# Performance work log

Hardware: AMD Instinct MI355X
Metric: run time of the kernel (lower is better)

Reference implementation:

```python
import jax, jax.numpy as jnp
import numpy as np

B, N, DIM = 8, 4096, 512
H, DH = 8, 64
INNER = H * DH
MIN_FREQ = 1.0 / 64
SCALE = 1.0
ROT_DIM = DH // 2  # 32, per spatial axis
EPS = 1e-5


def setup_inputs() -> dict:
    key = jax.random.key(0)
    ks = jax.random.split(key, 6)
    x = jax.random.normal(ks[0], (B, N, DIM), dtype=jnp.float32)
    pos = jax.random.uniform(ks[1], (B, N, 2), dtype=jnp.float32)
    W_qkv = jax.random.normal(ks[2], (3 * INNER, DIM), dtype=jnp.float32) * (1.0 / DH)
    gamma_k = jnp.ones((DH,), jnp.float32)
    beta_k = jnp.zeros((DH,), jnp.float32)
    gamma_v = jnp.ones((DH,), jnp.float32)
    beta_v = jnp.zeros((DH,), jnp.float32)
    W_out = jax.random.normal(ks[3], (DIM, INNER), dtype=jnp.float32) * (1.0 / np.sqrt(INNER))
    b_out = jnp.zeros((DIM,), jnp.float32)
    return {"x": x, "pos": pos, "W_qkv": W_qkv, "gamma_k": gamma_k, "beta_k": beta_k,
            "gamma_v": gamma_v, "beta_v": beta_v, "W_out": W_out, "b_out": b_out}


def _layernorm(t, gamma, beta):
    mu = jnp.mean(t, axis=-1, keepdims=True)
    var = jnp.var(t, axis=-1, keepdims=True)
    return (t - mu) * jax.lax.rsqrt(var + EPS) * gamma + beta


def _rotate_half(t):
    # '... (j d) -> ... j d' with j=2, then cat(-x2, x1)
    d = t.shape[-1] // 2
    x1, x2 = t[..., :d], t[..., d:]
    return jnp.concatenate((-x2, x1), axis=-1)


def _apply_rot(t, freqs):
    return t * jnp.cos(freqs) + _rotate_half(t) * jnp.sin(freqs)


def _freqs(coord):
    # coord: [b, n]; inv_freq over rotary half-dim
    inv_freq = 1.0 / (10000.0 ** (jnp.arange(0, ROT_DIM, 2, dtype=jnp.float32) / ROT_DIM))
    t = coord * (SCALE / MIN_FREQ)
    f = t[..., None] * inv_freq  # [b, n, ROT_DIM//2]
    return jnp.concatenate((f, f), axis=-1)[:, None, :, :]  # [b, 1, n, ROT_DIM]


def reference(x, pos, W_qkv, gamma_k, beta_k, gamma_v, beta_v, W_out, b_out):
    b, n, _ = x.shape
    qkv = x @ W_qkv.T  # [b, n, 3*INNER]
    q, k, v = jnp.split(qkv, 3, axis=-1)
    split = lambda t: t.reshape(b, n, H, DH).transpose(0, 2, 1, 3)  # b h n d
    q, k, v = split(q), split(k), split(v)

    # Galerkin: LayerNorm on K and V over head dim
    k = _layernorm(k, gamma_k, beta_k)
    v = _layernorm(v, gamma_v, beta_v)

    # 2D rotary on q, k: first half of head dim uses x-coords, second half y-coords
    fx, fy = _freqs(pos[..., 0]), _freqs(pos[..., 1])
    rot2d = lambda t: jnp.concatenate(
        (_apply_rot(t[..., :ROT_DIM], fx), _apply_rot(t[..., ROT_DIM:], fy)), axis=-1)
    q = rot2d(q)
    k = rot2d(k)

    # Associative linear attention: (K^T V) then Q @ (.) / n
    dots = jnp.einsum('bhnd,bhne->bhde', k, v)  # [b, h, d, d]
    out = jnp.einsum('bhnd,bhde->bhne', q, dots) * (1.0 / n)
    out = out.transpose(0, 2, 1, 3).reshape(b, n, INNER)
    return out @ W_out.T + b_out
```

## Files before the change

### kernel.cpp

```cpp
#include <hip/hip_runtime.h>
#include <math.h>

#define NB 8
#define NN 4096
#define NDIM 512
#define NH 8
#define NDH 64
#define QKVC 1536
#define NROWS (NB * NN)
#define EPSF 1e-5f
#define INV_N (1.0f / 4096.0f)
#define L2_10K_16 0.8304820237218406f

typedef __bf16 bf16x8_t __attribute__((ext_vector_type(8)));
typedef float f32x4_t __attribute__((ext_vector_type(4)));
typedef unsigned short u16x8 __attribute__((ext_vector_type(8)));

__device__ inline unsigned short f2bf(float f) {
    unsigned u = __builtin_bit_cast(unsigned, f);
    u += 0x7fff + ((u >> 16) & 1);
    return (unsigned short)(u >> 16);
}
__device__ inline float bf2f(unsigned short u) {
    unsigned v = (unsigned)u << 16;
    return __builtin_bit_cast(float, v);
}

#define GLOAD_LDS16(g, s) __builtin_amdgcn_global_load_lds(                    \
    (const __attribute__((address_space(1))) void*)(g),                        \
    (__attribute__((address_space(3))) void*)(s), 16, 0, 0)

__global__ __launch_bounds__(256)
void cvt_bf16_kernel(const float* __restrict__ s, unsigned short* __restrict__ d, int n)
{
    const int i = (blockIdx.x * 256 + threadIdx.x) * 8;
    if (i >= n) return;
    float4 a = *(const float4*)(s + i);
    float4 b = *(const float4*)(s + i + 4);
    ushort4 lo, hi;
    lo.x = f2bf(a.x); lo.y = f2bf(a.y); lo.z = f2bf(a.z); lo.w = f2bf(a.w);
    hi.x = f2bf(b.x); hi.y = f2bf(b.y); hi.z = f2bf(b.z); hi.w = f2bf(b.w);
    *(ushort4*)(d + i)     = lo;
    *(ushort4*)(d + i + 4) = hi;
}

__global__ __launch_bounds__(256)
void cvt_dots_kernel(const float* __restrict__ s, unsigned short* __restrict__ d)
{
    const int i = (blockIdx.x * 256 + threadIdx.x) * 4;
    float4 a = *(const float4*)(s + i);
    ushort4 o;
    o.x = f2bf(a.x * INV_N); o.y = f2bf(a.y * INV_N);
    o.z = f2bf(a.z * INV_N); o.w = f2bf(a.w * INV_N);
    *(ushort4*)(d + i) = o;
}

__global__ __launch_bounds__(512, 2)
void gemm_qkv_fused(const unsigned short* __restrict__ A,
                    const unsigned short* __restrict__ Bm,
                    const float* __restrict__ pos,
                    const float* __restrict__ gk, const float* __restrict__ bk,
                    const float* __restrict__ gv, const float* __restrict__ bvv,
                    unsigned short* __restrict__ qkvb)
{
    __shared__ __align__(16) unsigned short lds[2 * 32768];

    const int tid  = threadIdx.x;
    const int wave = tid >> 6;
    const int lane = tid & 63;

    int flat = blockIdx.y * 6 + blockIdx.x;
    flat = (flat & 7) * 96 + (flat >> 3);
    const int bx = flat % 6;
    const int by = flat / 6;
    const int m0 = by * 256;
    const int n0 = bx * 256;

    const int warp_m = wave >> 2;
    const int warp_n = wave & 3;
    const int fr = lane & 15;
    const int fq = lane >> 4;
    const int ch0 = ((fq ^ (fr & 7)) << 3);
    const int ch1 = ch0 ^ 32;

    const int r6 = tid >> 3;
    const int cs = (((tid & 7) ^ (r6 & 7)) << 3);
    const unsigned short* Asrc = A  + (size_t)(m0 + r6) * NDIM + cs;
    const unsigned short* Bsrc = Bm + (size_t)(n0 + (r6 >> 5) * 64 + (r6 & 31)) * NDIM + cs;
    const int sdst = wave * 512;

#define STG_A(tt, h, c) GLOAD_LDS16(Asrc + (size_t)((c) * 128 + (h) * 64) * NDIM + (tt) * 64, \
        &lds[(((tt) & 1) << 15) + ((h) << 13) + ((c) << 12) + sdst])
#define STG_B(tt, h, c) GLOAD_LDS16(Bsrc + (size_t)((c) * 128 + (h) * 32) * NDIM + (tt) * 64, \
        &lds[(((tt) & 1) << 15) + 16384 + ((h) << 13) + ((c) << 12) + sdst])
#define VMCNT4 asm volatile("s_waitcnt vmcnt(4)" ::: "memory")
#define BARF   { __builtin_amdgcn_s_barrier(); asm volatile("" ::: "memory"); }

    f32x4_t acc[8][4] = {};

    STG_A(0, 0, 0); STG_A(0, 0, 1);
    STG_B(0, 0, 0); STG_B(0, 0, 1);
    STG_B(0, 1, 0); STG_B(0, 1, 1);
    STG_A(0, 1, 0); STG_A(0, 1, 1);

    const unsigned short* Afr = &lds[(warp_m * 64 + fr) * 64];
    const unsigned short* Bfr = &lds[16384 + (warp_n * 32 + fr) * 64];

    bf16x8_t a0[4][2], a1[4][2], b0[2][2], b1[2][2];

    for (int tt = 0; tt < 7; ++tt) {
        const int rb = (tt & 1) << 15;
        VMCNT4; BARF;
        #pragma unroll
        for (int mi = 0; mi < 4; ++mi) {
            a0[mi][0] = *(const bf16x8_t*)&Afr[rb + mi * 1024 + ch0];
            a0[mi][1] = *(const bf16x8_t*)&Afr[rb + mi * 1024 + ch1];
        }
        #pragma unroll
        for (int nj = 0; nj < 2; ++nj) {
            b0[nj][0] = *(const bf16x8_t*)&Bfr[rb + nj * 1024 + ch0];
            b0[nj][1] = *(const bf16x8_t*)&Bfr[rb + nj * 1024 + ch1];
        }
        STG_A(tt + 1, 0, 0); STG_A(tt + 1, 0, 1);
        __builtin_amdgcn_s_setprio(1);
        #pragma unroll
        for (int mi = 0; mi < 4; ++mi)
            #pragma unroll
            for (int nj = 0; nj < 2; ++nj) {
                acc[mi][nj] = __builtin_amdgcn_mfma_f32_16x16x32_bf16(a0[mi][0], b0[nj][0], acc[mi][nj], 0, 0, 0);
                acc[mi][nj] = __builtin_amdgcn_mfma_f32_16x16x32_bf16(a0[mi][1], b0[nj][1], acc[mi][nj], 0, 0, 0);
            }
        __builtin_amdgcn_s_setprio(0);
        VMCNT4; BARF;
        #pragma unroll
        for (int nj = 0; nj < 2; ++nj) {
            b1[nj][0] = *(const bf16x8_t*)&Bfr[rb + 8192 + nj * 1024 + ch0];
            b1[nj][1] = *(const bf16x8_t*)&Bfr[rb + 8192 + nj * 1024 + ch1];
        }
        STG_B(tt + 1, 0, 0); STG_B(tt + 1, 0, 1);
        __builtin_amdgcn_s_setprio(1);
        #pragma unroll
        for (int mi = 0; mi < 4; ++mi)
            #pragma unroll
            for (int nj = 0; nj < 2; ++nj) {
                acc[mi][2 + nj] = __builtin_amdgcn_mfma_f32_16x16x32_bf16(a0[mi][0], b1[nj][0], acc[mi][2 + nj], 0, 0, 0);
                acc[mi][2 + nj] = __builtin_amdgcn_mfma_f32_16x16x32_bf16(a0[mi][1], b1[nj][1], acc[mi][2 + nj], 0, 0, 0);
            }
        __builtin_amdgcn_s_setprio(0);
        VMCNT4; BARF;
        #pragma unroll
        for (int mi = 0; mi < 4; ++mi) {
            a1[mi][0] = *(const bf16x8_t*)&Afr[rb + 8192 + mi * 1024 + ch0];
            a1[mi][1] = *(const bf16x8_t*)&Afr[rb + 8192 + mi * 1024 + ch1];
        }
        STG_B(tt + 1, 1, 0); STG_B(tt + 1, 1, 1);
        __builtin_amdgcn_s_setprio(1);
        #pragma unroll
        for (int mi = 0; mi < 4; ++mi)
            #pragma unroll
            for (int nj = 0; nj < 2; ++nj) {
                acc[4 + mi][nj] = __builtin_amdgcn_mfma_f32_16x16x32_bf16(a1[mi][0], b0[nj][0], acc[4 + mi][nj], 0, 0, 0);
                acc[4 + mi][nj] = __builtin_amdgcn_mfma_f32_16x16x32_bf16(a1[mi][1], b0[nj][1], acc[4 + mi][nj], 0, 0, 0);
            }
        __builtin_amdgcn_s_setprio(0);
        STG_A(tt + 1, 1, 0); STG_A(tt + 1, 1, 1);
        __builtin_amdgcn_s_setprio(1);
        #pragma unroll
        for (int mi = 0; mi < 4; ++mi)
            #pragma unroll
            for (int nj = 0; nj < 2; ++nj) {
                acc[4 + mi][2 + nj] = __builtin_amdgcn_mfma_f32_16x16x32_bf16(a1[mi][0], b1[nj][0], acc[4 + mi][2 + nj], 0, 0, 0);
                acc[4 + mi][2 + nj] = __builtin_amdgcn_mfma_f32_16x16x32_bf16(a1[mi][1], b1[nj][1], acc[4 + mi][2 + nj], 0, 0, 0);
            }
        __builtin_amdgcn_s_setprio(0);
    }
    {
        const int rb = 32768;
        asm volatile("s_waitcnt vmcnt(0)" ::: "memory");
        BARF;
        #pragma unroll
        for (int mi = 0; mi < 4; ++mi) {
            a0[mi][0] = *(const bf16x8_t*)&Afr[rb + mi * 1024 + ch0];
            a0[mi][1] = *(const bf16x8_t*)&Afr[rb + mi * 1024 + ch1];
        }
        #pragma unroll
        for (int nj = 0; nj < 2; ++nj) {
            b0[nj][0] = *(const bf16x8_t*)&Bfr[rb + nj * 1024 + ch0];
            b0[nj][1] = *(const bf16x8_t*)&Bfr[rb + nj * 1024 + ch1];
        }
        #pragma unroll
        for (int mi = 0; mi < 4; ++mi)
            #pragma unroll
            for (int nj = 0; nj < 2; ++nj) {
                acc[mi][nj] = __builtin_amdgcn_mfma_f32_16x16x32_bf16(a0[mi][0], b0[nj][0], acc[mi][nj], 0, 0, 0);
                acc[mi][nj] = __builtin_amdgcn_mfma_f32_16x16x32_bf16(a0[mi][1], b0[nj][1], acc[mi][nj], 0, 0, 0);
            }
        #pragma unroll
        for (int nj = 0; nj < 2; ++nj) {
            b1[nj][0] = *(const bf16x8_t*)&Bfr[rb + 8192 + nj * 1024 + ch0];
            b1[nj][1] = *(const bf16x8_t*)&Bfr[rb + 8192 + nj * 1024 + ch1];
        }
        #pragma unroll
        for (int mi = 0; mi < 4; ++mi)
            #pragma unroll
            for (int nj = 0; nj < 2; ++nj) {
                acc[mi][2 + nj] = __builtin_amdgcn_mfma_f32_16x16x32_bf16(a0[mi][0], b1[nj][0], acc[mi][2 + nj], 0, 0, 0);
                acc[mi][2 + nj] = __builtin_amdgcn_mfma_f32_16x16x32_bf16(a0[mi][1], b1[nj][1], acc[mi][2 + nj], 0, 0, 0);
            }
        #pragma unroll
        for (int mi = 0; mi < 4; ++mi) {
            a1[mi][0] = *(const bf16x8_t*)&Afr[rb + 8192 + mi * 1024 + ch0];
            a1[mi][1] = *(const bf16x8_t*)&Afr[rb + 8192 + mi * 1024 + ch1];
        }
        #pragma unroll
        for (int mi = 0; mi < 4; ++mi)
            #pragma unroll
            for (int nj = 0; nj < 2; ++nj) {
                acc[4 + mi][nj] = __builtin_amdgcn_mfma_f32_16x16x32_bf16(a1[mi][0], b0[nj][0], acc[4 + mi][nj], 0, 0, 0);
                acc[4 + mi][nj] = __builtin_amdgcn_mfma_f32_16x16x32_bf16(a1[mi][1], b0[nj][1], acc[4 + mi][nj], 0, 0, 0);
                acc[4 + mi][2 + nj] = __builtin_amdgcn_mfma_f32_16x16x32_bf16(a1[mi][0], b1[nj][0], acc[4 + mi][2 + nj], 0, 0, 0);
                acc[4 + mi][2 + nj] = __builtin_amdgcn_mfma_f32_16x16x32_bf16(a1[mi][1], b1[nj][1], acc[4 + mi][2 + nj], 0, 0, 0);
            }
    }
#undef STG_A
#undef STG_B
#undef VMCNT4
#undef BARF

    const int type = (n0 + warp_n * 64) >> 9;
    const int c  = lane & 15;
    const int g4 = (lane >> 4) * 4;
    const int mrow0 = m0 + warp_m * 128;

    if (type != 0) {
        const float* gamma = (type == 1) ? gk : gv;
        const float* beta  = (type == 1) ? bk : bvv;
        float gm[4], bt[4];
        #pragma unroll
        for (int j = 0; j < 4; ++j) { gm[j] = gamma[j * 16 + c]; bt[j] = beta[j * 16 + c]; }
        #pragma unroll
        for (int i = 0; i < 8; ++i)
            #pragma unroll
            for (int r = 0; r < 4; ++r) {
                float t0 = acc[i][0][r], t1 = acc[i][1][r];
                float t2 = acc[i][2][r], t3 = acc[i][3][r];
                float s  = t0 + t1 + t2 + t3;
                float ss = t0*t0 + t1*t1 + t2*t2 + t3*t3;
                #pragma unroll
                for (int msk = 1; msk < 16; msk <<= 1) {
                    s  += __shfl_xor(s,  msk, 64);
                    ss += __shfl_xor(ss, msk, 64);
                }
                const float mu = s * (1.0f / 64.0f);
                const float rs = rsqrtf(ss * (1.0f / 64.0f) - mu * mu + EPSF);
                acc[i][0][r] = (t0 - mu) * rs * gm[0] + bt[0];
                acc[i][1][r] = (t1 - mu) * rs * gm[1] + bt[1];
                acc[i][2][r] = (t2 - mu) * rs * gm[2] + bt[2];
                acc[i][3][r] = (t3 - mu) * rs * gm[3] + bt[3];
            }
    }
    if (type != 2) {
        const float Kc = 64.0f * exp2f(-(float)c * L2_10K_16);
        #pragma unroll
        for (int i = 0; i < 8; ++i)
            #pragma unroll
            for (int r = 0; r < 4; ++r) {
                const int row = mrow0 + (i >> 2) * 64 + (i & 3) * 16 + g4 + r;
                const float2 p = ((const float2*)pos)[row];
                float sx, cx, sy, cy;
                __sincosf(p.x * Kc, &sx, &cx);
                __sincosf(p.y * Kc, &sy, &cy);
                const float t0 = acc[i][0][r], t1 = acc[i][1][r];
                const float t2 = acc[i][2][r], t3 = acc[i][3][r];
                acc[i][0][r] = t0 * cx - t1 * sx;
                acc[i][1][r] = t1 * cx + t0 * sx;
                acc[i][2][r] = t2 * cy - t3 * sy;
                acc[i][3][r] = t3 * cy + t2 * sy;
            }
    }
    #pragma unroll
    for (int i = 0; i < 8; ++i)
        #pragma unroll
        for (int j = 0; j < 4; ++j) {
            unsigned short* qp = qkvb
                + (size_t)(mrow0 + (i >> 2) * 64 + (i & 3) * 16 + g4) * QKVC
                + n0 + warp_n * 64 + j * 16 + c;
            #pragma unroll
            for (int r = 0; r < 4; ++r)
                qp[(size_t)r * QKVC] = f2bf(acc[i][j][r]);
        }
}

__global__ __launch_bounds__(256)
void dots_kernel(const unsigned short* __restrict__ qkvb, float* __restrict__ dots)
{
    __shared__ float ks[32][64];
    __shared__ float vs[32][64];
    const int b = blockIdx.z, h = blockIdx.y;
    const int n0 = blockIdx.x * 512;
    const int t = threadIdx.x;
    const int row = t >> 3;
    const int c8  = (t & 7) * 8;
    const int d0 = (t >> 4) * 4;
    const int e0 = (t & 15) * 4;

    float acc[4][4] = {{0.0f}};
    const size_t kbase = (size_t)(b * NN + n0 + row) * QKVC + 512 + h * NDH + c8;
    const size_t vbase = kbase + 512;

    u16x8 ku = *(const u16x8*)(qkvb + kbase);
    u16x8 vu = *(const u16x8*)(qkvb + vbase);

    for (int s = 0; s < 16; ++s) {
        __syncthreads();
        #pragma unroll
        for (int j = 0; j < 8; ++j) {
            ks[row][c8 + j] = bf2f(ku[j]);
            vs[row][c8 + j] = bf2f(vu[j]);
        }
        __syncthreads();
        if (s + 1 < 16) {
            ku = *(const u16x8*)(qkvb + kbase + (size_t)(s + 1) * 32 * QKVC);
            vu = *(const u16x8*)(qkvb + vbase + (size_t)(s + 1) * 32 * QKVC);
        }
        #pragma unroll
        for (int r = 0; r < 32; ++r) {
            float4 kd = *(float4*)&ks[r][d0];
            float4 ve = *(float4*)&vs[r][e0];
            acc[0][0] += kd.x*ve.x; acc[0][1] += kd.x*ve.y; acc[0][2] += kd.x*ve.z; acc[0][3] += kd.x*ve.w;
            acc[1][0] += kd.y*ve.x; acc[1][1] += kd.y*ve.y; acc[1][2] += kd.y*ve.z; acc[1][3] += kd.y*ve.w;
            acc[2][0] += kd.z*ve.x; acc[2][1] += kd.z*ve.y; acc[2][2] += kd.z*ve.z; acc[2][3] += kd.z*ve.w;
            acc[3][0] += kd.w*ve.x; acc[3][1] += kd.w*ve.y; acc[3][2] += kd.w*ve.z; acc[3][3] += kd.w*ve.w;
        }
    }
    float* dp = dots + ((size_t)(b * NH + h) * 64 + d0) * 64 + e0;
    #pragma unroll
    for (int i = 0; i < 4; ++i)
        #pragma unroll
        for (int j = 0; j < 4; ++j)
            atomicAdd(dp + i * 64 + j, acc[i][j]);
}

__global__ __launch_bounds__(256)
void dotsw_mfma(const unsigned short* __restrict__ Woutb,
                const unsigned short* __restrict__ dots_bf,
                unsigned short* __restrict__ M2b)
{
    __shared__ unsigned short As[128 * 64];
    __shared__ unsigned short Bs[64 * 64];
    const int t = threadIdx.x;
    const int wave = t >> 6;
    const int lane = t & 63;
    const int dp0 = blockIdx.x * 128;
    const int h = blockIdx.y, b = blockIdx.z;

    const int srow = lane >> 3;
    const int scol = (lane & 7) * 8;
    const unsigned short* Ag = Woutb + (size_t)(dp0 + wave * 32 + srow) * NDIM
                             + h * NDH + scol;
    const unsigned short* Bg = dots_bf + ((size_t)(b * NH + h) * 64 + wave * 16 + srow) * 64
                             + scol;
    #pragma unroll
    for (int i = 0; i < 4; ++i)
        GLOAD_LDS16(Ag + (size_t)i * 8 * NDIM, As + wave * 2048 + i * 512);
    #pragma unroll
    for (int i = 0; i < 2; ++i)
        GLOAD_LDS16(Bg + (size_t)i * 8 * 64, Bs + wave * 1024 + i * 512);
    __syncthreads();

    const int wm = (wave >> 1) * 64;
    const int wn = (wave & 1) * 32;
    const int fr = lane & 15;
    const int fq = (lane >> 4) * 8;

    f32x4_t acc[4][2] = {};
    #pragma unroll
    for (int kk = 0; kk < 2; ++kk) {
        bf16x8_t af[4], bf[2];
        #pragma unroll
        for (int i = 0; i < 4; ++i)
            af[i] = *(const bf16x8_t*)&As[(wm + i * 16 + fr) * 64 + kk * 32 + fq];
        #pragma unroll
        for (int j = 0; j < 2; ++j)
            bf[j] = *(const bf16x8_t*)&Bs[(wn + j * 16 + fr) * 64 + kk * 32 + fq];
        #pragma unroll
        for (int i = 0; i < 4; ++i)
            #pragma unroll
            for (int j = 0; j < 2; ++j)
                acc[i][j] = __builtin_amdgcn_mfma_f32_16x16x32_bf16(
                    af[i], bf[j], acc[i][j], 0, 0, 0);
    }

    const int c  = lane & 15;
    const int g4 = (lane >> 4) * 4;
    #pragma unroll
    for (int i = 0; i < 4; ++i)
        #pragma unroll
        for (int j = 0; j < 2; ++j) {
            unsigned short* mp = M2b + ((size_t)(b * NDIM) + dp0 + wm + i * 16 + g4) * NDIM
                               + h * NDH + wn + j * 16 + c;
            #pragma unroll
            for (int r = 0; r < 4; ++r)
                mp[(size_t)r * NDIM] = f2bf(acc[i][j][r]);
        }
}

__global__ __launch_bounds__(256)
void gemm_out_mfma(const unsigned short* __restrict__ qkvb,
                   const unsigned short* __restrict__ M2b,
                   const float* __restrict__ bias, float* __restrict__ C)
{
    __shared__ unsigned short As[128 * 32];
    __shared__ unsigned short Bs[128 * 32];
    const int t    = threadIdx.x;
    const int wave = t >> 6;
    const int lane = t & 63;
    const int b  = blockIdx.z;
    const int m0 = b * NN + blockIdx.y * 128;
    const int n0 = blockIdx.x * 128;
    const int wm = (wave >> 1) * 64;
    const int wn = (wave & 1) * 64;
    const int K = NDIM;

    f32x4_t acc[4][4] = {};

    const int srow = wave * 32 + (lane >> 2);
    const int scol = (lane & 3) * 8;
    const unsigned short* Ag = qkvb + (size_t)(m0 + srow) * QKVC + scol;
    const unsigned short* Bg = M2b + ((size_t)b * NDIM + n0 + srow) * NDIM + scol;
    unsigned short* sA = As + wave * 1024;
    unsigned short* sB = Bs + wave * 1024;

    const int fr = lane & 15;
    const int fq = (lane >> 4) * 8;

    for (int kt = 0; kt < K; kt += 32) {
        __syncthreads();
        GLOAD_LDS16(Ag + kt,             sA);
        GLOAD_LDS16(Ag + kt + (size_t)16 * QKVC, sA + 512);
        GLOAD_LDS16(Bg + kt,             sB);
        GLOAD_LDS16(Bg + kt + 16 * NDIM, sB + 512);
        __syncthreads();

        bf16x8_t af[4], bf[4];
        #pragma unroll
        for (int i = 0; i < 4; ++i) {
            af[i] = *(const bf16x8_t*)&As[(wm + i * 16 + fr) * 32 + fq];
            bf[i] = *(const bf16x8_t*)&Bs[(wn + i * 16 + fr) * 32 + fq];
        }
        #pragma unroll
        for (int i = 0; i < 4; ++i)
            #pragma unroll
            for (int j = 0; j < 4; ++j)
                acc[i][j] = __builtin_amdgcn_mfma_f32_16x16x32_bf16(
                    af[i], bf[j], acc[i][j], 0, 0, 0);
    }

    const int crow = (lane >> 4) * 4;
    const int ccol = lane & 15;
    #pragma unroll
    for (int j = 0; j < 4; ++j) {
        const int cn = n0 + wn + j * 16 + ccol;
        const float bb = bias[cn];
        #pragma unroll
        for (int i = 0; i < 4; ++i) {
            float* cp = C + (size_t)(m0 + wm + i * 16 + crow) * NDIM + cn;
            #pragma unroll
            for (int r = 0; r < 4; ++r)
                cp[(size_t)r * NDIM] = acc[i][j][r] + bb;
        }
    }
}

extern "C" void kernel_launch(void* const* d_in, const int* in_sizes, int n_in,
                              void* d_out, int out_size, void* d_ws, size_t ws_size,
                              hipStream_t stream)
{
    const float* x    = (const float*)d_in[0];
    const float* pos  = (const float*)d_in[1];
    const float* Wqkv = (const float*)d_in[2];
    const float* gk   = (const float*)d_in[3];
    const float* bk   = (const float*)d_in[4];
    const float* gv   = (const float*)d_in[5];
    const float* bv   = (const float*)d_in[6];
    const float* Wout = (const float*)d_in[7];
    const float* bout = (const float*)d_in[8];
    float* out = (float*)d_out;

    float* dots = (float*)d_ws;
    unsigned short* dots_bf = (unsigned short*)(dots + (size_t)NB * NH * 64 * 64);
    unsigned short* M2b     = dots_bf + (size_t)NB * NH * 64 * 64;
    unsigned short* qkvb    = M2b + (size_t)NB * NDIM * NDIM;
    unsigned short* xb      = qkvb + (size_t)NROWS * QKVC;
    unsigned short* Wqkvb   = xb + (size_t)NROWS * NDIM;
    unsigned short* Woutb   = Wqkvb + (size_t)QKVC * NDIM;

    hipMemsetAsync(dots, 0, (size_t)NB * NH * 64 * 64 * sizeof(float), stream);

    dim3 blk(256);
    cvt_bf16_kernel<<<dim3(NROWS * NDIM / 2048), blk, 0, stream>>>(x, xb, NROWS * NDIM);
    cvt_bf16_kernel<<<dim3(QKVC * NDIM / 2048), blk, 0, stream>>>(Wqkv, Wqkvb, QKVC * NDIM);
    cvt_bf16_kernel<<<dim3(NDIM * NDIM / 2048), blk, 0, stream>>>(Wout, Woutb, NDIM * NDIM);
    gemm_qkv_fused<<<dim3(QKVC / 256, NROWS / 256), dim3(512), 0, stream>>>(
        xb, Wqkvb, pos, gk, bk, gv, bv, qkvb);
    dots_kernel<<<dim3(NN / 512, NH, NB), blk, 0, stream>>>(qkvb, dots);
    cvt_dots_kernel<<<dim3(NB * NH * 64 * 64 / 1024), blk, 0, stream>>>(dots, dots_bf);
    dotsw_mfma<<<dim3(NDIM / 128, NH, NB), blk, 0, stream>>>(Woutb, dots_bf, M2b);
    gemm_out_mfma<<<dim3(NDIM / 128, NN / 128, NB), blk, 0, stream>>>(
        qkvb, M2b, bout, out);
}
```

Before: 321.6 us.

## Store K/V transposed from QKV GEMM and compute K^T V with MFMA

The QKV GEMM epilogue now writes Q to its own contiguous buffer and K and V into per-head transposed layouts ([b,h,d,n]). The scalar-FMA dots kernel, which converted bf16 to fp32 in shared memory, is replaced by a double-buffered MFMA kernel that streams the transposed K/V tiles into XOR-swizzled LDS. The goal is to move the K^T V reduction onto matrix cores and make its loads contiguous. In exchange, the epilogue's transposed stores are strided 8-byte writes across N, which may cost some write efficiency in the GEMM.

```diff
diff --git a/kernel.cpp b/kernel.cpp
--- a/kernel.cpp
+++ b/kernel.cpp
@@ -61,7 +61,9 @@
                     const float* __restrict__ pos,
                     const float* __restrict__ gk, const float* __restrict__ bk,
                     const float* __restrict__ gv, const float* __restrict__ bvv,
-                    unsigned short* __restrict__ qkvb)
+                    unsigned short* __restrict__ qb,
+                    unsigned short* __restrict__ kT,
+                    unsigned short* __restrict__ vT)
 {
     __shared__ __align__(16) unsigned short lds[2 * 32768];
 
@@ -227,7 +229,8 @@
 #undef VMCNT4
 #undef BARF
 
-    const int type = (n0 + warp_n * 64) >> 9;
+    const int nc = n0 + warp_n * 64;
+    const int type = nc >> 9;
     const int c  = lane & 15;
     const int g4 = (lane >> 4) * 4;
     const int mrow0 = m0 + warp_m * 128;
@@ -278,67 +281,110 @@
                 acc[i][3][r] = t3 * cy + t2 * sy;
             }
     }
+    if (type == 0) {
+        #pragma unroll
+        for (int i = 0; i < 8; ++i)
+            #pragma unroll
+            for (int j = 0; j < 4; ++j) {
+                unsigned short* qp = qb
+                    + (size_t)(mrow0 + (i >> 2) * 64 + (i & 3) * 16 + g4) * NDIM
+                    + nc + j * 16 + c;
+                #pragma unroll
+                for (int r = 0; r < 4; ++r)
+                    qp[(size_t)r * NDIM] = f2bf(acc[i][j][r]);
+            }
+    } else {
+        unsigned short* T = (type == 1) ? kT : vT;
+        const int h = (nc >> 6) & 7;
+        #pragma unroll
+        for (int i = 0; i < 8; ++i) {
+            const int row = mrow0 + (i >> 2) * 64 + (i & 3) * 16 + g4;
+            const int bb = row >> 12;
+            const int nl = row & 4095;
+            #pragma unroll
+            for (int j = 0; j < 4; ++j) {
+                ushort4 o;
+                o.x = f2bf(acc[i][j][0]); o.y = f2bf(acc[i][j][1]);
+                o.z = f2bf(acc[i][j][2]); o.w = f2bf(acc[i][j][3]);
+                *(ushort4*)(T + ((size_t)((bb * NH + h) * 64 + j * 16 + c)) * NN + nl) = o;
+            }
+        }
+    }
+}
+
+__global__ __launch_bounds__(256)
+void dots_mfma(const unsigned short* __restrict__ kT,
+               const unsigned short* __restrict__ vT,
+               float* __restrict__ dots)
+{
+    __shared__ __align__(16) unsigned short sk[2][64 * 64];
+    __shared__ __align__(16) unsigned short sv[2][64 * 64];
+    const int t = threadIdx.x;
+    const int w = t >> 6, l = t & 63;
+    const int bh = blockIdx.z * NH + blockIdx.y;
+    const int n0 = blockIdx.x * 512;
+
+    const int r8 = l >> 3;
+    const int cs = ((l & 7) ^ r8) * 8;
+    const unsigned short* ksrc = kT + (size_t)(bh * 64 + w * 16 + r8) * NN + n0 + cs;
+    const unsigned short* vsrc = vT + (size_t)(bh * 64 + w * 16 + r8) * NN + n0 + cs;
+
+#define STGK(buf, kt, q) GLOAD_LDS16(ksrc + (size_t)(q) * 8 * NN + (kt), \
+        &sk[buf][w * 1024 + (q) * 512])
+#define STGV(buf, kt, q) GLOAD_LDS16(vsrc + (size_t)(q) * 8 * NN + (kt), \
+        &sv[buf][w * 1024 + (q) * 512])
+
+    const int fr = l & 15, fq = l >> 4;
+    const int doff = (w >> 1) * 32, eoff = (w & 1) * 32;
+
+    f32x4_t acc[2][2] = {};
+
+    STGK(0, 0, 0); STGK(0, 0, 1); STGV(0, 0, 0); STGV(0, 0, 1);
+
+    for (int s = 0; s < 8; ++s) {
+        const int buf = s & 1;
+        asm volatile("s_waitcnt vmcnt(0)" ::: "memory");
+        __builtin_amdgcn_s_barrier();
+        bf16x8_t ak[2][2], bv[2][2];
+        #pragma unroll
+        for (int di = 0; di < 2; ++di)
+            #pragma unroll
+            for (int ks = 0; ks < 2; ++ks)
+                ak[di][ks] = *(const bf16x8_t*)
+                    &sk[buf][(doff + di * 16 + fr) * 64 + (((ks * 4 + fq) ^ (fr & 7)) * 8)];
+        #pragma unroll
+        for (int ej = 0; ej < 2; ++ej)
+            #pragma unroll
+            for (int ks = 0; ks < 2; ++ks)
+                bv[ej][ks] = *(const bf16x8_t*)
+                    &sv[buf][(eoff + ej * 16 + fr) * 64 + (((ks * 4 + fq) ^ (fr & 7)) * 8)];
+        if (s + 1 < 8) {
+            const int nb = buf ^ 1, kt = (s + 1) * 64;
+            STGK(nb, kt, 0); STGK(nb, kt, 1); STGV(nb, kt, 0); STGV(nb, kt, 1);
+        }
+        #pragma unroll
+        for (int ks = 0; ks < 2; ++ks)
+            #pragma unroll
+            for (int di = 0; di < 2; ++di)
+                #pragma unroll
+                for (int ej = 0; ej < 2; ++ej)
+                    acc[di][ej] = __builtin_amdgcn_mfma_f32_16x16x32_bf16(
+                        ak[di][ks], bv[ej][ks], acc[di][ej], 0, 0, 0);
+    }
+#undef STGK
+#undef STGV
+
+    float* dp = dots + (size_t)bh * 64 * 64;
+    const int cc = l & 15;
+    const int rr = (l >> 4) * 4;
     #pragma unroll
-    for (int i = 0; i < 8; ++i)
-        #pragma unroll
-        for (int j = 0; j < 4; ++j) {
-            unsigned short* qp = qkvb
-                + (size_t)(mrow0 + (i >> 2) * 64 + (i & 3) * 16 + g4) * QKVC
-                + n0 + warp_n * 64 + j * 16 + c;
+    for (int di = 0; di < 2; ++di)
+        #pragma unroll
+        for (int ej = 0; ej < 2; ++ej)
             #pragma unroll
             for (int r = 0; r < 4; ++r)
-                qp[(size_t)r * QKVC] = f2bf(acc[i][j][r]);
-        }
-}
-
-__global__ __launch_bounds__(256)
-void dots_kernel(const unsigned short* __restrict__ qkvb, float* __restrict__ dots)
-{
-    __shared__ float ks[32][64];
-    __shared__ float vs[32][64];
-    const int b = blockIdx.z, h = blockIdx.y;
-    const int n0 = blockIdx.x * 512;
-    const int t = threadIdx.x;
-    const int row = t >> 3;
-    const int c8  = (t & 7) * 8;
-    const int d0 = (t >> 4) * 4;
-    const int e0 = (t & 15) * 4;
-
-    float acc[4][4] = {{0.0f}};
-    const size_t kbase = (size_t)(b * NN + n0 + row) * QKVC + 512 + h * NDH + c8;
-    const size_t vbase = kbase + 512;
-
-    u16x8 ku = *(const u16x8*)(qkvb + kbase);
-    u16x8 vu = *(const u16x8*)(qkvb + vbase);
-
-    for (int s = 0; s < 16; ++s) {
-        __syncthreads();
-        #pragma unroll
-        for (int j = 0; j < 8; ++j) {
-            ks[row][c8 + j] = bf2f(ku[j]);
-            vs[row][c8 + j] = bf2f(vu[j]);
-        }
-        __syncthreads();
-        if (s + 1 < 16) {
-            ku = *(const u16x8*)(qkvb + kbase + (size_t)(s + 1) * 32 * QKVC);
-            vu = *(const u16x8*)(qkvb + vbase + (size_t)(s + 1) * 32 * QKVC);
-        }
-        #pragma unroll
-        for (int r = 0; r < 32; ++r) {
-            float4 kd = *(float4*)&ks[r][d0];
-            float4 ve = *(float4*)&vs[r][e0];
-            acc[0][0] += kd.x*ve.x; acc[0][1] += kd.x*ve.y; acc[0][2] += kd.x*ve.z; acc[0][3] += kd.x*ve.w;
-            acc[1][0] += kd.y*ve.x; acc[1][1] += kd.y*ve.y; acc[1][2] += kd.y*ve.z; acc[1][3] += kd.y*ve.w;
-            acc[2][0] += kd.z*ve.x; acc[2][1] += kd.z*ve.y; acc[2][2] += kd.z*ve.z; acc[2][3] += kd.z*ve.w;
-            acc[3][0] += kd.w*ve.x; acc[3][1] += kd.w*ve.y; acc[3][2] += kd.w*ve.z; acc[3][3] += kd.w*ve.w;
-        }
-    }
-    float* dp = dots + ((size_t)(b * NH + h) * 64 + d0) * 64 + e0;
-    #pragma unroll
-    for (int i = 0; i < 4; ++i)
-        #pragma unroll
-        for (int j = 0; j < 4; ++j)
-            atomicAdd(dp + i * 64 + j, acc[i][j]);
+                atomicAdd(dp + (doff + di * 16 + rr + r) * 64 + eoff + ej * 16 + cc,
+                          acc[di][ej][r]);
 }
 
 __global__ __launch_bounds__(256)
@@ -406,7 +452,7 @@
 }
 
 __global__ __launch_bounds__(256)
-void gemm_out_mfma(const unsigned short* __restrict__ qkvb,
+void gemm_out_mfma(const unsigned short* __restrict__ qb,
                    const unsigned short* __restrict__ M2b,
                    const float* __restrict__ bias, float* __restrict__ C)
 {
@@ -426,7 +472,7 @@
 
     const int srow = wave * 32 + (lane >> 2);
     const int scol = (lane & 3) * 8;
-    const unsigned short* Ag = qkvb + (size_t)(m0 + srow) * QKVC + scol;
+    const unsigned short* Ag = qb + (size_t)(m0 + srow) * NDIM + scol;
     const unsigned short* Bg = M2b + ((size_t)b * NDIM + n0 + srow) * NDIM + scol;
     unsigned short* sA = As + wave * 1024;
     unsigned short* sB = Bs + wave * 1024;
@@ -437,7 +483,7 @@
     for (int kt = 0; kt < K; kt += 32) {
         __syncthreads();
         GLOAD_LDS16(Ag + kt,             sA);
-        GLOAD_LDS16(Ag + kt + (size_t)16 * QKVC, sA + 512);
+        GLOAD_LDS16(Ag + kt + 16 * NDIM, sA + 512);
         GLOAD_LDS16(Bg + kt,             sB);
         GLOAD_LDS16(Bg + kt + 16 * NDIM, sB + 512);
         __syncthreads();
@@ -490,8 +536,10 @@
     float* dots = (float*)d_ws;
     unsigned short* dots_bf = (unsigned short*)(dots + (size_t)NB * NH * 64 * 64);
     unsigned short* M2b     = dots_bf + (size_t)NB * NH * 64 * 64;
-    unsigned short* qkvb    = M2b + (size_t)NB * NDIM * NDIM;
-    unsigned short* xb      = qkvb + (size_t)NROWS * QKVC;
+    unsigned short* qb      = M2b + (size_t)NB * NDIM * NDIM;
+    unsigned short* kT      = qb + (size_t)NROWS * NDIM;
+    unsigned short* vT      = kT + (size_t)NB * NH * NDH * NN;
+    unsigned short* xb      = vT + (size_t)NB * NH * NDH * NN;
     unsigned short* Wqkvb   = xb + (size_t)NROWS * NDIM;
     unsigned short* Woutb   = Wqkvb + (size_t)QKVC * NDIM;
 
@@ -502,10 +550,10 @@
     cvt_bf16_kernel<<<dim3(QKVC * NDIM / 2048), blk, 0, stream>>>(Wqkv, Wqkvb, QKVC * NDIM);
     cvt_bf16_kernel<<<dim3(NDIM * NDIM / 2048), blk, 0, stream>>>(Wout, Woutb, NDIM * NDIM);
     gemm_qkv_fused<<<dim3(QKVC / 256, NROWS / 256), dim3(512), 0, stream>>>(
-        xb, Wqkvb, pos, gk, bk, gv, bv, qkvb);
-    dots_kernel<<<dim3(NN / 512, NH, NB), blk, 0, stream>>>(qkvb, dots);
+        xb, Wqkvb, pos, gk, bk, gv, bv, qb, kT, vT);
+    dots_mfma<<<dim3(NN / 512, NH, NB), blk, 0, stream>>>(kT, vT, dots);
     cvt_dots_kernel<<<dim3(NB * NH * 64 * 64 / 1024), blk, 0, stream>>>(dots, dots_bf);
     dotsw_mfma<<<dim3(NDIM / 128, NH, NB), blk, 0, stream>>>(Woutb, dots_bf, M2b);
     gemm_out_mfma<<<dim3(NDIM / 128, NN / 128, NB), blk, 0, stream>>>(
-        qkvb, M2b, bout, out);
-}
+        qb, M2b, bout, out);
+}
```

Measured after the change: 285.7 us. 1.13x faster.
